# Kernel optimization log

Measured on AMD Instinct MI355X. Metric: run time of the kernel, lower is better.

## Reference

```python
import jax, jax.numpy as jnp
import numpy as np

FEATURE_DIM = 128

def setup_inputs() -> dict:
    key0 = jax.random.key(0)
    k1, k2, k3 = jax.random.split(key0, 3)
    B, NQ, NK, D = 4, 4096, 4096, FEATURE_DIM
    return {
        "target": jax.random.normal(k1, (B, NQ, D), dtype=jnp.float32),
        "key": jax.random.normal(k2, (B, NK, D), dtype=jnp.float32),
        "value": jax.random.normal(k3, (B, NK, D), dtype=jnp.float32),
    }

def reference(target, key, value):
    # Lan_K F: scores = target @ key^T / sqrt(d); weights = softmax(scores); out = weights @ value
    scale = 1.0 / np.sqrt(FEATURE_DIM).astype(np.float32)
    scores = jnp.einsum('bqd,bkd->bqk', target, key) * scale  # [B, NQ, NK]
    weights = jax.nn.softmax(scores, axis=-1)
    return jnp.einsum('bqk,bkd->bqd', weights, value)  # [B, NQ, D]
```

## Files before the change

### kernel.cpp

```cpp
#include <hip/hip_runtime.h>
#include <stdint.h>

#define B_ 4
#define NQ_ 4096
#define NK_ 4096
#define D_ 128
#define BM_ 64
#define BN_ 128
#define NITER_ (NK_/BN_)
#define OS_ 66

typedef __attribute__((ext_vector_type(8))) short short8;
typedef __attribute__((ext_vector_type(4))) float floatx4;
typedef unsigned int u32;

union frag_u { u32 u[4]; short8 s; };

__device__ __forceinline__ unsigned short f2bf_rne(float x){
  union { float f; u32 u; } c; c.f = x;
  u32 u = c.u;
  return (unsigned short)((u + 0x7fffu + ((u >> 16) & 1u)) >> 16);
}
__device__ __forceinline__ u32 pk2bf(float a, float b){
  union { float f; u32 u; } x, y; x.f = a; y.f = b;
  return ((x.u + 0x8000u) >> 16) | ((y.u + 0x8000u) & 0xffff0000u);
}

__global__ __launch_bounds__(256) void prep_kernel(
    const float* __restrict__ k, const float* __restrict__ v,
    unsigned short* __restrict__ kf, unsigned short* __restrict__ vf){
  __shared__ __align__(16) char smem[40960];
  const int t = threadIdx.x;
  const int blk = blockIdx.x;
  if (blk < 128){
    int b = blk >> 5, it = blk & 31;
    const float* src = k + ((size_t)b*NK_ + it*BN_)*D_;
    #pragma unroll
    for (int i = 0; i < 16; i++){
      int f = t + i*256;
      int row = f >> 5, c4 = f & 31;
      float4 a = *(const float4*)(src + (size_t)row*D_ + c4*4);
      ushort4 s;
      s.x = f2bf_rne(a.x); s.y = f2bf_rne(a.y);
      s.z = f2bf_rne(a.z); s.w = f2bf_rne(a.w);
      int kg = row >> 5, rem = row & 31;
      int dh = (rem >> 2) & 1;
      int l15 = ((rem >> 3) << 2) | (rem & 3);
      int wq = kg*2 + dh;
      int j = c4 >> 3, l4 = (c4 >> 1) & 3, half = c4 & 1;
      *(ushort4*)(smem + (wq*4 + j)*1088 + l4*272 + l15*16 + half*8) = s;
    }
    __syncthreads();
    unsigned short* dst = kf + (size_t)(b*32 + it)*2048*8;
    #pragma unroll
    for (int i = 0; i < 8; i++){
      int c = t + i*256;
      int lane = c & 63, j = (c >> 6) & 3, wq = c >> 8;
      int l15 = lane & 15, l4 = lane >> 4;
      short8 x = *(const short8*)(smem + (wq*4 + j)*1088 + l4*272 + l15*16);
      *(short8*)(dst + (size_t)c*8) = x;
    }
  } else {
    int blk2 = blk - 128;
    int b = blk2 >> 5, it = blk2 & 31;
    const float* src = v + ((size_t)b*NK_ + it*BN_)*D_;
    #pragma unroll
    for (int i = 0; i < 16; i++){
      int f = t + i*256;
      int row = f >> 5, c4 = f & 31;
      float4 a = *(const float4*)(src + (size_t)row*D_ + c4*4);
      float vals[4] = {a.x, a.y, a.z, a.w};
      int kk = row & 7, l4a = (row >> 3) & 3, kga = row >> 5;
      #pragma unroll
      for (int jj = 0; jj < 4; jj++){
        int d = c4*4 + jj;
        int dh = d >> 6, dt = (d >> 4) & 3, l15 = d & 15;
        int c = ((kga*2 + dh)*4 + dt)*64 + l4a*16 + l15;
        *(unsigned short*)(smem + c*16 + (c>>2)*16 + kk*2) = f2bf_rne(vals[jj]);
      }
    }
    __syncthreads();
    unsigned short* dst = vf + (size_t)(b*32 + it)*2048*8;
    #pragma unroll
    for (int i = 0; i < 8; i++){
      int c = t + i*256;
      short8 x = *(const short8*)(smem + c*16 + (c>>2)*16);
      *(short8*)(dst + (size_t)c*8) = x;
    }
  }
}

__global__ __launch_bounds__(512) void attn_kernel(
    const float* __restrict__ Qf, const unsigned short* __restrict__ Kb,
    const unsigned short* __restrict__ Vt, float* __restrict__ Out){
  __shared__ __align__(16) char sm[69632];
  float* smO = (float*)sm;
  float* smL = (float*)(sm + 67584);

  const int bi = blockIdx.x;
  const int b  = (bi >> 1) & 3;
  const int qt = ((bi >> 3) << 1) | (bi & 1);
  const int q0 = qt * BM_;
  const int tid = threadIdx.x;
  const int w = tid >> 6, lane = tid & 63;
  const int kg = w >> 1, dh = w & 1;
  const int l15 = lane & 15, l4 = lane >> 4;

  const short8* Kfrag = (const short8*)Kb;
  const short8* Vfrag = (const short8*)Vt;
  const size_t FSTRIDE = 8*4*64;
  const size_t kbase0 = ((size_t)b*256 + kg*2 + 0)*256 + lane;
  const size_t kbase1 = ((size_t)b*256 + kg*2 + 1)*256 + lane;
  const size_t vbase  = ((size_t)b*256 + w)*256 + lane;

  short8 qf[4][4];
  {
    const float* qp = Qf + ((size_t)b*NQ_ + q0)*D_;
    #pragma unroll
    for (int nb = 0; nb < 4; nb++)
      #pragma unroll
      for (int kbq = 0; kbq < 4; kbq++){
        const float* p = qp + (size_t)(nb*16 + l15)*D_ + kbq*32 + l4*8;
        float4 a = *(const float4*)p;
        float4 c4 = *(const float4*)(p + 4);
        frag_u f;
        f.u[0] = pk2bf(a.x, a.y);  f.u[1] = pk2bf(a.z, a.w);
        f.u[2] = pk2bf(c4.x, c4.y); f.u[3] = pk2bf(c4.z, c4.w);
        qf[nb][kbq] = f.s;
      }
  }

  short8 kf[2][4], vf[4];
  #pragma unroll
  for (int j = 0; j < 4; j++){
    kf[0][j] = Kfrag[kbase0 + j*64];
    kf[1][j] = Kfrag[kbase1 + j*64];
  }
  #pragma unroll
  for (int dt = 0; dt < 4; dt++) vf[dt] = Vfrag[vbase + dt*64];

  floatx4 o[4][4];
  #pragma unroll
  for (int nb = 0; nb < 4; nb++)
    #pragma unroll
    for (int dt = 0; dt < 4; dt++) o[nb][dt] = (floatx4)0.0f;
  float lsum[4] = {0.f, 0.f, 0.f, 0.f};

  const float SL = 0.08838834764831845f * 1.4426950408889634f;

  for (int it = 0; it < NITER_; ++it){
    floatx4 s0[4], s1[4];
    #pragma unroll
    for (int nb = 0; nb < 4; nb++){
      s0[nb] = (floatx4)0.0f; s1[nb] = (floatx4)0.0f;
      s0[nb] = __builtin_amdgcn_mfma_f32_16x16x32_bf16(kf[0][0], qf[nb][0], s0[nb],0,0,0);
      s0[nb] = __builtin_amdgcn_mfma_f32_16x16x32_bf16(kf[0][1], qf[nb][1], s0[nb],0,0,0);
      s0[nb] = __builtin_amdgcn_mfma_f32_16x16x32_bf16(kf[0][2], qf[nb][2], s0[nb],0,0,0);
      s0[nb] = __builtin_amdgcn_mfma_f32_16x16x32_bf16(kf[0][3], qf[nb][3], s0[nb],0,0,0);
      s1[nb] = __builtin_amdgcn_mfma_f32_16x16x32_bf16(kf[1][0], qf[nb][0], s1[nb],0,0,0);
      s1[nb] = __builtin_amdgcn_mfma_f32_16x16x32_bf16(kf[1][1], qf[nb][1], s1[nb],0,0,0);
      s1[nb] = __builtin_amdgcn_mfma_f32_16x16x32_bf16(kf[1][2], qf[nb][2], s1[nb],0,0,0);
      s1[nb] = __builtin_amdgcn_mfma_f32_16x16x32_bf16(kf[1][3], qf[nb][3], s1[nb],0,0,0);
    }
    if (it + 1 < NITER_){
      #pragma unroll
      for (int j = 0; j < 4; j++){
        kf[0][j] = Kfrag[kbase0 + (size_t)(it+1)*FSTRIDE + j*64];
        kf[1][j] = Kfrag[kbase1 + (size_t)(it+1)*FSTRIDE + j*64];
      }
    }
    #pragma unroll
    for (int nb = 0; nb < 4; nb++){
      float p0 = __builtin_amdgcn_exp2f(s0[nb][0] * SL);
      float p1 = __builtin_amdgcn_exp2f(s0[nb][1] * SL);
      float p2 = __builtin_amdgcn_exp2f(s0[nb][2] * SL);
      float p3 = __builtin_amdgcn_exp2f(s0[nb][3] * SL);
      float p4 = __builtin_amdgcn_exp2f(s1[nb][0] * SL);
      float p5 = __builtin_amdgcn_exp2f(s1[nb][1] * SL);
      float p6 = __builtin_amdgcn_exp2f(s1[nb][2] * SL);
      float p7 = __builtin_amdgcn_exp2f(s1[nb][3] * SL);
      lsum[nb] += ((p0 + p1) + (p2 + p3)) + ((p4 + p5) + (p6 + p7));
      frag_u pf;
      pf.u[0] = pk2bf(p0, p1); pf.u[1] = pk2bf(p2, p3);
      pf.u[2] = pk2bf(p4, p5); pf.u[3] = pk2bf(p6, p7);
      o[nb][0] = __builtin_amdgcn_mfma_f32_16x16x32_bf16(pf.s, vf[0], o[nb][0],0,0,0);
      o[nb][1] = __builtin_amdgcn_mfma_f32_16x16x32_bf16(pf.s, vf[1], o[nb][1],0,0,0);
      o[nb][2] = __builtin_amdgcn_mfma_f32_16x16x32_bf16(pf.s, vf[2], o[nb][2],0,0,0);
      o[nb][3] = __builtin_amdgcn_mfma_f32_16x16x32_bf16(pf.s, vf[3], o[nb][3],0,0,0);
    }
    if (it + 1 < NITER_){
      #pragma unroll
      for (int dt = 0; dt < 4; dt++)
        vf[dt] = Vfrag[vbase + (size_t)(it+1)*FSTRIDE + dt*64];
    }
  }

  #pragma unroll
  for (int nb = 0; nb < 4; nb++){
    float v = lsum[nb];
    v += __shfl_xor(v, 16);
    v += __shfl_xor(v, 32);
    lsum[nb] = v;
  }
  if (l4 == 0)
    #pragma unroll
    for (int nb = 0; nb < 4; nb++)
      smL[w*64 + nb*16 + l15] = lsum[nb];

  __syncthreads();

  if (w >= 4){
    float* r = smO + (size_t)(w - 4) * 4224;
    #pragma unroll
    for (int nb = 0; nb < 4; nb++)
      #pragma unroll
      for (int dt = 0; dt < 4; dt++)
        #pragma unroll
        for (int q = 0; q < 4; q++)
          r[(size_t)(nb*16 + l4*4 + q)*OS_ + dt*16 + l15] = o[nb][dt][q];
  }
  __syncthreads();
  if (w < 4){
    float* r = smO + (size_t)w * 4224;
    #pragma unroll
    for (int nb = 0; nb < 4; nb++)
      #pragma unroll
      for (int dt = 0; dt < 4; dt++)
        #pragma unroll
        for (int q = 0; q < 4; q++)
          o[nb][dt][q] += r[(size_t)(nb*16 + l4*4 + q)*OS_ + dt*16 + l15];
  }
  __syncthreads();
  if (w == 2 || w == 3){
    float* r = smO + (size_t)(w - 2) * 4224;
    #pragma unroll
    for (int nb = 0; nb < 4; nb++)
      #pragma unroll
      for (int dt = 0; dt < 4; dt++)
        #pragma unroll
        for (int q = 0; q < 4; q++)
          r[(size_t)(nb*16 + l4*4 + q)*OS_ + dt*16 + l15] = o[nb][dt][q];
  }
  __syncthreads();
  if (w < 2){
    float* r = smO + (size_t)w * 4224;
    float* og = Out + ((size_t)b*NQ_ + q0)*D_ + dh*64;
    #pragma unroll
    for (int nb = 0; nb < 4; nb++)
      #pragma unroll
      for (int q = 0; q < 4; q++){
        int row = nb*16 + l4*4 + q;
        float lt = 0.f;
        #pragma unroll
        for (int w2 = 0; w2 < 8; w2++) lt += smL[w2*64 + row];
        float inv = 2.0f / lt;
        #pragma unroll
        for (int dt = 0; dt < 4; dt++){
          float val = o[nb][dt][q] + r[(size_t)row*OS_ + dt*16 + l15];
          og[(size_t)row*D_ + dt*16 + l15] = val * inv;
        }
      }
  }
}

extern "C" void kernel_launch(void* const* d_in, const int* in_sizes, int n_in,
                              void* d_out, int out_size, void* d_ws, size_t ws_size,
                              hipStream_t stream){
  const float* q = (const float*)d_in[0];
  const float* k = (const float*)d_in[1];
  const float* v = (const float*)d_in[2];
  float* out = (float*)d_out;
  unsigned short* kb = (unsigned short*)d_ws;
  unsigned short* vt = kb + (size_t)B_*NK_*D_;
  prep_kernel<<<256, 256, 0, stream>>>(k, v, kb, vt);
  attn_kernel<<<256, 512, 0, stream>>>(q, kb, vt, out);
}
```

Measured before the change: 131.4 us.

## Split score computation across waves and share P via LDS with smaller query tiles

Halves the query tile to 32 rows and doubles the grid to 512 blocks. Previously each pair of waves sharing a key group recomputed the same QK^T scores. Now each wave computes a distinct 16-key score slice, and the bf16 probabilities are exchanged through a double-buffered LDS tile so each wave can do its PV MFMAs over the full 32-key chunk. This removes the redundant score MFMAs and exp work and raises block count and occupancy (launch_bounds 512,4, smaller LDS). The cost is an LDS round trip plus a workgroup barrier on every key iteration.

```diff
diff --git a/kernel.cpp b/kernel.cpp
--- a/kernel.cpp
+++ b/kernel.cpp
@@ -5,9 +5,10 @@
 #define NQ_ 4096
 #define NK_ 4096
 #define D_ 128
-#define BM_ 64
+#define BM_ 32
 #define BN_ 128
 #define NITER_ (NK_/BN_)
+#define PS_ 136
 #define OS_ 66
 
 typedef __attribute__((ext_vector_type(8))) short short8;
@@ -15,6 +16,7 @@
 typedef unsigned int u32;
 
 union frag_u { u32 u[4]; short8 s; };
+union pair_u { u32 u[2]; uint2 v; };
 
 __device__ __forceinline__ unsigned short f2bf_rne(float x){
   union { float f; u32 u; } c; c.f = x;
@@ -90,12 +92,13 @@
   }
 }
 
-__global__ __launch_bounds__(512) void attn_kernel(
+__global__ __launch_bounds__(512, 4) void attn_kernel(
     const float* __restrict__ Qf, const unsigned short* __restrict__ Kb,
     const unsigned short* __restrict__ Vt, float* __restrict__ Out){
-  __shared__ __align__(16) char sm[69632];
+  __shared__ __align__(16) char sm[34816];
+  unsigned short* smP = (unsigned short*)sm;
   float* smO = (float*)sm;
-  float* smL = (float*)(sm + 67584);
+  float* smL = (float*)(sm + 33792);
 
   const int bi = blockIdx.x;
   const int b  = (bi >> 1) & 3;
@@ -109,15 +112,13 @@
   const short8* Kfrag = (const short8*)Kb;
   const short8* Vfrag = (const short8*)Vt;
   const size_t FSTRIDE = 8*4*64;
-  const size_t kbase0 = ((size_t)b*256 + kg*2 + 0)*256 + lane;
-  const size_t kbase1 = ((size_t)b*256 + kg*2 + 1)*256 + lane;
-  const size_t vbase  = ((size_t)b*256 + w)*256 + lane;
-
-  short8 qf[4][4];
+  const size_t fbase = ((size_t)b*256 + w)*256 + lane;
+
+  short8 qf[2][4];
   {
     const float* qp = Qf + ((size_t)b*NQ_ + q0)*D_;
     #pragma unroll
-    for (int nb = 0; nb < 4; nb++)
+    for (int nb = 0; nb < 2; nb++)
       #pragma unroll
       for (int kbq = 0; kbq < 4; kbq++){
         const float* p = qp + (size_t)(nb*16 + l15)*D_ + kbq*32 + l4*8;
@@ -130,73 +131,68 @@
       }
   }
 
-  short8 kf[2][4], vf[4];
-  #pragma unroll
-  for (int j = 0; j < 4; j++){
-    kf[0][j] = Kfrag[kbase0 + j*64];
-    kf[1][j] = Kfrag[kbase1 + j*64];
-  }
-  #pragma unroll
-  for (int dt = 0; dt < 4; dt++) vf[dt] = Vfrag[vbase + dt*64];
-
-  floatx4 o[4][4];
-  #pragma unroll
-  for (int nb = 0; nb < 4; nb++)
+  short8 kf[4], vf[4];
+  #pragma unroll
+  for (int j = 0; j < 4; j++) kf[j] = Kfrag[fbase + j*64];
+  #pragma unroll
+  for (int dt = 0; dt < 4; dt++) vf[dt] = Vfrag[fbase + dt*64];
+
+  floatx4 o[2][4];
+  #pragma unroll
+  for (int nb = 0; nb < 2; nb++)
     #pragma unroll
     for (int dt = 0; dt < 4; dt++) o[nb][dt] = (floatx4)0.0f;
-  float lsum[4] = {0.f, 0.f, 0.f, 0.f};
+  float lsum[2] = {0.f, 0.f};
 
   const float SL = 0.08838834764831845f * 1.4426950408889634f;
+  const size_t prow = (size_t)kg*32 + l4*8;
 
   for (int it = 0; it < NITER_; ++it){
-    floatx4 s0[4], s1[4];
-    #pragma unroll
-    for (int nb = 0; nb < 4; nb++){
-      s0[nb] = (floatx4)0.0f; s1[nb] = (floatx4)0.0f;
-      s0[nb] = __builtin_amdgcn_mfma_f32_16x16x32_bf16(kf[0][0], qf[nb][0], s0[nb],0,0,0);
-      s0[nb] = __builtin_amdgcn_mfma_f32_16x16x32_bf16(kf[0][1], qf[nb][1], s0[nb],0,0,0);
-      s0[nb] = __builtin_amdgcn_mfma_f32_16x16x32_bf16(kf[0][2], qf[nb][2], s0[nb],0,0,0);
-      s0[nb] = __builtin_amdgcn_mfma_f32_16x16x32_bf16(kf[0][3], qf[nb][3], s0[nb],0,0,0);
-      s1[nb] = __builtin_amdgcn_mfma_f32_16x16x32_bf16(kf[1][0], qf[nb][0], s1[nb],0,0,0);
-      s1[nb] = __builtin_amdgcn_mfma_f32_16x16x32_bf16(kf[1][1], qf[nb][1], s1[nb],0,0,0);
-      s1[nb] = __builtin_amdgcn_mfma_f32_16x16x32_bf16(kf[1][2], qf[nb][2], s1[nb],0,0,0);
-      s1[nb] = __builtin_amdgcn_mfma_f32_16x16x32_bf16(kf[1][3], qf[nb][3], s1[nb],0,0,0);
+    floatx4 s[2];
+    #pragma unroll
+    for (int nb = 0; nb < 2; nb++){
+      s[nb] = (floatx4)0.0f;
+      s[nb] = __builtin_amdgcn_mfma_f32_16x16x32_bf16(kf[0], qf[nb][0], s[nb], 0,0,0);
+      s[nb] = __builtin_amdgcn_mfma_f32_16x16x32_bf16(kf[1], qf[nb][1], s[nb], 0,0,0);
+      s[nb] = __builtin_amdgcn_mfma_f32_16x16x32_bf16(kf[2], qf[nb][2], s[nb], 0,0,0);
+      s[nb] = __builtin_amdgcn_mfma_f32_16x16x32_bf16(kf[3], qf[nb][3], s[nb], 0,0,0);
     }
     if (it + 1 < NITER_){
       #pragma unroll
-      for (int j = 0; j < 4; j++){
-        kf[0][j] = Kfrag[kbase0 + (size_t)(it+1)*FSTRIDE + j*64];
-        kf[1][j] = Kfrag[kbase1 + (size_t)(it+1)*FSTRIDE + j*64];
-      }
-    }
-    #pragma unroll
-    for (int nb = 0; nb < 4; nb++){
-      float p0 = __builtin_amdgcn_exp2f(s0[nb][0] * SL);
-      float p1 = __builtin_amdgcn_exp2f(s0[nb][1] * SL);
-      float p2 = __builtin_amdgcn_exp2f(s0[nb][2] * SL);
-      float p3 = __builtin_amdgcn_exp2f(s0[nb][3] * SL);
-      float p4 = __builtin_amdgcn_exp2f(s1[nb][0] * SL);
-      float p5 = __builtin_amdgcn_exp2f(s1[nb][1] * SL);
-      float p6 = __builtin_amdgcn_exp2f(s1[nb][2] * SL);
-      float p7 = __builtin_amdgcn_exp2f(s1[nb][3] * SL);
-      lsum[nb] += ((p0 + p1) + (p2 + p3)) + ((p4 + p5) + (p6 + p7));
-      frag_u pf;
-      pf.u[0] = pk2bf(p0, p1); pf.u[1] = pk2bf(p2, p3);
-      pf.u[2] = pk2bf(p4, p5); pf.u[3] = pk2bf(p6, p7);
-      o[nb][0] = __builtin_amdgcn_mfma_f32_16x16x32_bf16(pf.s, vf[0], o[nb][0],0,0,0);
-      o[nb][1] = __builtin_amdgcn_mfma_f32_16x16x32_bf16(pf.s, vf[1], o[nb][1],0,0,0);
-      o[nb][2] = __builtin_amdgcn_mfma_f32_16x16x32_bf16(pf.s, vf[2], o[nb][2],0,0,0);
-      o[nb][3] = __builtin_amdgcn_mfma_f32_16x16x32_bf16(pf.s, vf[3], o[nb][3],0,0,0);
+      for (int j = 0; j < 4; j++)
+        kf[j] = Kfrag[fbase + (size_t)(it+1)*FSTRIDE + j*64];
+    }
+    unsigned short* smPb = smP + (it & 1) * (32 * PS_);
+    #pragma unroll
+    for (int nb = 0; nb < 2; nb++){
+      float p0 = __builtin_amdgcn_exp2f(s[nb][0] * SL);
+      float p1 = __builtin_amdgcn_exp2f(s[nb][1] * SL);
+      float p2 = __builtin_amdgcn_exp2f(s[nb][2] * SL);
+      float p3 = __builtin_amdgcn_exp2f(s[nb][3] * SL);
+      lsum[nb] += (p0 + p1) + (p2 + p3);
+      pair_u pp; pp.u[0] = pk2bf(p0, p1); pp.u[1] = pk2bf(p2, p3);
+      *(uint2*)(smPb + (size_t)(nb*16 + l15)*PS_ + prow + dh*4) = pp.v;
+    }
+    asm volatile("s_waitcnt lgkmcnt(0)" ::: "memory");
+    __builtin_amdgcn_s_barrier();
+    asm volatile("" ::: "memory");
+    #pragma unroll
+    for (int nb = 0; nb < 2; nb++){
+      short8 pf = *(const short8*)(smPb + (size_t)(nb*16 + l15)*PS_ + prow);
+      o[nb][0] = __builtin_amdgcn_mfma_f32_16x16x32_bf16(pf, vf[0], o[nb][0], 0,0,0);
+      o[nb][1] = __builtin_amdgcn_mfma_f32_16x16x32_bf16(pf, vf[1], o[nb][1], 0,0,0);
+      o[nb][2] = __builtin_amdgcn_mfma_f32_16x16x32_bf16(pf, vf[2], o[nb][2], 0,0,0);
+      o[nb][3] = __builtin_amdgcn_mfma_f32_16x16x32_bf16(pf, vf[3], o[nb][3], 0,0,0);
     }
     if (it + 1 < NITER_){
       #pragma unroll
       for (int dt = 0; dt < 4; dt++)
-        vf[dt] = Vfrag[vbase + (size_t)(it+1)*FSTRIDE + dt*64];
-    }
-  }
-
-  #pragma unroll
-  for (int nb = 0; nb < 4; nb++){
+        vf[dt] = Vfrag[fbase + (size_t)(it+1)*FSTRIDE + dt*64];
+    }
+  }
+
+  #pragma unroll
+  for (int nb = 0; nb < 2; nb++){
     float v = lsum[nb];
     v += __shfl_xor(v, 16);
     v += __shfl_xor(v, 32);
@@ -204,15 +200,15 @@
   }
   if (l4 == 0)
     #pragma unroll
-    for (int nb = 0; nb < 4; nb++)
-      smL[w*64 + nb*16 + l15] = lsum[nb];
+    for (int nb = 0; nb < 2; nb++)
+      smL[w*32 + nb*16 + l15] = lsum[nb];
 
   __syncthreads();
 
   if (w >= 4){
-    float* r = smO + (size_t)(w - 4) * 4224;
-    #pragma unroll
-    for (int nb = 0; nb < 4; nb++)
+    float* r = smO + (size_t)(w - 4) * 2112;
+    #pragma unroll
+    for (int nb = 0; nb < 2; nb++)
       #pragma unroll
       for (int dt = 0; dt < 4; dt++)
         #pragma unroll
@@ -221,9 +217,9 @@
   }
   __syncthreads();
   if (w < 4){
-    float* r = smO + (size_t)w * 4224;
-    #pragma unroll
-    for (int nb = 0; nb < 4; nb++)
+    float* r = smO + (size_t)w * 2112;
+    #pragma unroll
+    for (int nb = 0; nb < 2; nb++)
       #pragma unroll
       for (int dt = 0; dt < 4; dt++)
         #pragma unroll
@@ -232,9 +228,9 @@
   }
   __syncthreads();
   if (w == 2 || w == 3){
-    float* r = smO + (size_t)(w - 2) * 4224;
-    #pragma unroll
-    for (int nb = 0; nb < 4; nb++)
+    float* r = smO + (size_t)(w - 2) * 2112;
+    #pragma unroll
+    for (int nb = 0; nb < 2; nb++)
       #pragma unroll
       for (int dt = 0; dt < 4; dt++)
         #pragma unroll
@@ -243,17 +239,17 @@
   }
   __syncthreads();
   if (w < 2){
-    float* r = smO + (size_t)w * 4224;
+    float* r = smO + (size_t)w * 2112;
     float* og = Out + ((size_t)b*NQ_ + q0)*D_ + dh*64;
     #pragma unroll
-    for (int nb = 0; nb < 4; nb++)
+    for (int nb = 0; nb < 2; nb++)
       #pragma unroll
       for (int q = 0; q < 4; q++){
         int row = nb*16 + l4*4 + q;
         float lt = 0.f;
         #pragma unroll
-        for (int w2 = 0; w2 < 8; w2++) lt += smL[w2*64 + row];
-        float inv = 2.0f / lt;
+        for (int w2 = 0; w2 < 8; w2++) lt += smL[w2*32 + row];
+        float inv = 1.0f / lt;
         #pragma unroll
         for (int dt = 0; dt < 4; dt++){
           float val = o[nb][dt][q] + r[(size_t)row*OS_ + dt*16 + l15];
@@ -273,5 +269,5 @@
   unsigned short* kb = (unsigned short*)d_ws;
   unsigned short* vt = kb + (size_t)B_*NK_*D_;
   prep_kernel<<<256, 256, 0, stream>>>(k, v, kb, vt);
-  attn_kernel<<<256, 512, 0, stream>>>(q, kb, vt, out);
-}
+  attn_kernel<<<512, 512, 0, stream>>>(q, kb, vt, out);
+}
```

After: 123.0 us. 6.4% less time.
